# Optimization experiments

Measured on AMD Instinct MI355X. Metric: run time of the kernel, lower is better.

## Reference

```python
import jax, jax.numpy as jnp
import numpy as np

B, N, H, D, L = 4, 1024, 8, 256, 4
SVD, NSP = 16, 512
DK = D // H
EPS = 1e-6


def setup_inputs() -> dict:
    key = jax.random.key(0)
    ks = jax.random.split(key, 40)
    p = {}
    p["x"] = jax.random.normal(ks[0], (B, N, D), jnp.float32)
    p["in_degrees"] = jax.random.randint(ks[1], (N,), 0, N)
    p["out_degrees"] = jax.random.randint(ks[2], (N,), 0, N)
    p["spatial_pos"] = jax.random.randint(ks[3], (N, N), 0, NSP)
    p["svd_emb"] = jax.random.normal(ks[4], (N, 2 * SVD), jnp.float32)
    # embedding tables (padding_idx=0 -> zero row)
    p["in_deg_emb"] = (0.02 * jax.random.normal(ks[5], (N, D), jnp.float32)).at[0].set(0.0)
    p["out_deg_emb"] = (0.02 * jax.random.normal(ks[6], (N, D), jnp.float32)).at[0].set(0.0)
    p["spatial_emb"] = (0.02 * jax.random.normal(ks[7], (NSP, H), jnp.float32)).at[0].set(0.0)
    # SVD linear (stored [in, out]; y = x @ W + b)
    p["W_svd"] = 0.02 * jax.random.normal(ks[8], (2 * SVD, D), jnp.float32)
    p["b_svd"] = jnp.zeros((D,), jnp.float32)
    # per-layer stacked transformer params
    names = ["Wq", "Wk", "Wv", "Wa", "W1", "W2"]
    for i, nm in enumerate(names):
        p[nm] = 0.05 * jax.random.normal(ks[9 + i], (L, D, D), jnp.float32)
    for nm in ["bq", "bk", "bv", "ba", "b1", "b2", "ln1_b", "ln2_b"]:
        p[nm] = jnp.zeros((L, D), jnp.float32)
    p["ln1_g"] = jnp.ones((L, D), jnp.float32)
    p["ln2_g"] = jnp.ones((L, D), jnp.float32)
    return p


def _ln(x, g, b):
    mu = jnp.mean(x, axis=-1, keepdims=True)
    var = jnp.mean(jnp.square(x - mu), axis=-1, keepdims=True)
    return (x - mu) * jax.lax.rsqrt(var + EPS) * g + b


def _forward(x, svd_emb, W_svd, b_svd, in_deg_emb, out_deg_emb, spatial_emb,
             Wq, bq, Wk, bk, Wv, bv, Wa, ba, ln1_g, ln1_b,
             W1, b1, W2, b2, ln2_g, ln2_b,
             in_degrees, out_degrees, spatial_pos):
    # node-level: degree embeddings ([N,D] broadcasts over batch)
    x = x + in_deg_emb[in_degrees] + out_deg_emb[out_degrees]
    # node-level: SVD embedding (deterministic sign = +1 -> concat(u, -v))
    pos = jnp.concatenate([svd_emb[:, :SVD], -svd_emb[:, SVD:]], axis=-1)
    x = x + pos @ W_svd + b_svd
    # attention-level spatial bias: [N,N,H] -> [H,N,N], broadcast over batch
    attn_bias = jnp.transpose(spatial_emb[spatial_pos], (2, 0, 1))
    scale = 1.0 / jnp.sqrt(jnp.asarray(DK, x.dtype))

    def body(h, params):
        wq, bq_, wk, bk_, wv, bv_, wa, ba_, g1, b1_, w1, bb1, w2, bb2, g2, b2_ = params
        q = (h @ wq + bq_).reshape(B, N, H, DK)
        k = (h @ wk + bk_).reshape(B, N, H, DK)
        v = (h @ wv + bv_).reshape(B, N, H, DK)
        # scores [B,H,N,N] + spatial bias [H,N,N]
        scores = jnp.einsum('bqhd,bkhd->bhqk', q, k) * scale + attn_bias
        attn = jax.nn.softmax(scores, axis=-1)
        o = jnp.einsum('bhqk,bkhd->bqhd', attn, v).reshape(B, N, D)
        h = _ln(h + o @ wa + ba_, g1, b1_)
        f = jnp.maximum(h @ w1 + bb1, 0.0) @ w2 + bb2
        h = _ln(h + f, g2, b2_)
        return h, None

    x, _ = jax.lax.scan(body, x, (Wq, bq, Wk, bk, Wv, bv, Wa, ba, ln1_g, ln1_b,
                                  W1, b1, W2, b2, ln2_g, ln2_b))
    return x


def reference(x, svd_emb, W_svd, b_svd, in_deg_emb, out_deg_emb, spatial_emb,
              Wq, bq, Wk, bk, Wv, bv, Wa, ba, ln1_g, ln1_b,
              W1, b1, W2, b2, ln2_g, ln2_b,
              in_degrees, out_degrees, spatial_pos):
    return _forward(x, svd_emb, W_svd, b_svd, in_deg_emb, out_deg_emb, spatial_emb,
                    Wq, bq, Wk, bk, Wv, bv, Wa, ba, ln1_g, ln1_b,
                    W1, b1, W2, b2, ln2_g, ln2_b,
                    in_degrees, out_degrees, spatial_pos)
```

## Files before the change

### kernel.cpp

```cpp
#include <hip/hip_runtime.h>
#include <hip/hip_bf16.h>
#include <math.h>

#define NN 1024
#define BB 4
#define HH 8
#define DD 256
#define LL 4
#define DKK 32
#define MM 4096
#define EPSF 1e-6f

typedef __attribute__((ext_vector_type(8))) short short8;
typedef __attribute__((ext_vector_type(4))) float f32x4;

__device__ __forceinline__ unsigned short f2bf(float f) {
    __hip_bfloat16 h = __float2bfloat16(f);
    return *(unsigned short*)&h;
}
__device__ __forceinline__ float bf2f(unsigned short u) {
    unsigned v = ((unsigned)u) << 16;
    return __builtin_bit_cast(float, v);
}

__global__ __launch_bounds__(256) void init_kernel(
    const float* __restrict__ x, const int* __restrict__ deg_in,
    const int* __restrict__ deg_out, const float* __restrict__ svd,
    const float* __restrict__ in_emb, const float* __restrict__ out_emb,
    const float* __restrict__ Wsvd, const float* __restrict__ bsvd,
    const float* __restrict__ Wq, const float* __restrict__ Wk,
    const float* __restrict__ Wv, const float* __restrict__ Wa,
    const float* __restrict__ W1, const float* __restrict__ W2,
    const int* __restrict__ sp, const float* __restrict__ spemb,
    float* __restrict__ h, short* __restrict__ hb,
    short* __restrict__ Wt, short* __restrict__ bsw)
{
    int blk = blockIdx.x;
    int tid = threadIdx.x;
    {
        int n = blk & (NN - 1);
        int di = deg_in[n], dou = deg_out[n];
        float acc = x[(size_t)blk * DD + tid] + in_emb[(size_t)di * DD + tid]
                  + out_emb[(size_t)dou * DD + tid] + bsvd[tid];
        const float* sv = &svd[n * 32];
#pragma unroll
        for (int j = 0; j < 32; ++j) {
            float v = sv[j];
            v = (j < 16) ? v : -v;
            acc += v * Wsvd[j * DD + tid];
        }
        h[(size_t)blk * DD + tid] = acc;
        hb[(size_t)blk * DD + tid] = (short)f2bf(acc);
    }
    if (blk < 384) {
        __shared__ float t[64][65];
        int z = blk >> 4, tile = blk & 15;
        int name = z >> 2;
        const float* srcs[6] = {Wq, Wk, Wv, Wa, W1, W2};
        const float* W = srcs[name] + (size_t)(z & 3) * DD * DD;
        short* dst = Wt + (size_t)z * DD * DD;
        int r0 = (tile >> 2) * 64, c0 = (tile & 3) * 64;
#pragma unroll
        for (int i = 0; i < 16; ++i) {
            int idx = i * 256 + tid;
            int r = idx >> 6, cc = idx & 63;
            t[r][cc] = W[(size_t)(r0 + r) * DD + c0 + cc];
        }
        __syncthreads();
#pragma unroll
        for (int i = 0; i < 16; ++i) {
            int idx = i * 256 + tid;
            int n = idx >> 6, k = idx & 63;
            dst[(size_t)(c0 + n) * DD + r0 + k] = (short)f2bf(t[k][n]);
        }
    } else if (blk < 640) {
        int tt = (blk - 384) * 256 + tid;
        int ln = tt & 63, kt = (tt >> 6) & 15, q16 = tt >> 10;
        int qd = ln >> 4, cc = ln & 15;
        unsigned buf[8][8];
#pragma unroll
        for (int j = 0; j < 16; ++j) {
            int f = j >> 2, r = j & 3;
            int row = q16 * 16 + qd * 4 + r;
            int col = kt * 64 + f * 16 + cc;
            int pp = sp[row * NN + col];
#pragma unroll
            for (int hh = 0; hh < 8; ++hh) {
                unsigned short u = f2bf(spemb[pp * 8 + hh]);
                if (j & 1) buf[hh][j >> 1] |= ((unsigned)u) << 16;
                else       buf[hh][j >> 1] = u;
            }
        }
#pragma unroll
        for (int hh = 0; hh < 8; ++hh) {
            uint4* dst = (uint4*)&bsw[(((size_t)hh * 64 + q16) * 16 + kt) * 1024 + (size_t)ln * 16];
            dst[0] = make_uint4(buf[hh][0], buf[hh][1], buf[hh][2], buf[hh][3]);
            dst[1] = make_uint4(buf[hh][4], buf[hh][5], buf[hh][6], buf[hh][7]);
        }
    }
}

__global__ __launch_bounds__(256) void gemm_qkv_kernel(
    const short* __restrict__ A,
    const short* __restrict__ Wtq, const short* __restrict__ Wtk,
    const short* __restrict__ Wtv,
    const float* __restrict__ bq, const float* __restrict__ bk,
    const float* __restrict__ bv,
    short* __restrict__ qo, short* __restrict__ ko, short* __restrict__ vo)
{
    int z = blockIdx.z;
    const short* Wt = (z == 0) ? Wtq : (z == 1) ? Wtk : Wtv;
    const float* bs = (z == 0) ? bq : (z == 1) ? bk : bv;
    int tid = threadIdx.x, wave = tid >> 6, lane = tid & 63;
    int quad = lane >> 4, c = lane & 15;
    int m0 = blockIdx.x * 16;
    int n0 = blockIdx.y * 64 + wave * 16;
    f32x4 acc = {0.f, 0.f, 0.f, 0.f};
    const short* Ap = &A[(size_t)(m0 + c) * DD];
#pragma unroll
    for (int ks = 0; ks < 8; ++ks) {
        short8 af = *(const short8*)&Ap[ks * 32 + quad * 8];
        short8 bf = *(const short8*)&Wt[(size_t)(n0 + c) * DD + ks * 32 + quad * 8];
        acc = __builtin_amdgcn_mfma_f32_16x16x32_bf16(af, bf, acc, 0, 0, 0);
    }
    int b = m0 >> 10;
    int tok0 = (m0 & (NN - 1)) + quad * 4;
    int col = n0 + c;
    int head = col >> 5, dk = col & 31;
    int bh = b * 8 + head;
    float bv2 = bs[col];
    const float scale = 0.17677669529663687f;
    if (z == 2) {
        ushort4 pk;
        pk.x = f2bf(acc[0] + bv2); pk.y = f2bf(acc[1] + bv2);
        pk.z = f2bf(acc[2] + bv2); pk.w = f2bf(acc[3] + bv2);
        *(ushort4*)&vo[((size_t)bh * DKK + dk) * NN + tok0] = pk;
    } else {
        short* out = (z == 0) ? qo : ko;
        float sc = (z == 0) ? scale : 1.0f;
#pragma unroll
        for (int r = 0; r < 4; ++r)
            out[((size_t)bh * NN + tok0 + r) * DKK + dk] =
                (short)f2bf((acc[r] + bv2) * sc);
    }
}

template <int QKV>
__global__ __launch_bounds__(512) void layer_kernel(
    const short* __restrict__ q, const short* __restrict__ k,
    const short* __restrict__ vt, const short* __restrict__ bsw,
    const short* __restrict__ Wta, const short* __restrict__ Wt1,
    const short* __restrict__ Wt2,
    const float* __restrict__ ba, const float* __restrict__ b1,
    const float* __restrict__ b2,
    const float* __restrict__ g1, const float* __restrict__ lb1,
    const float* __restrict__ g2, const float* __restrict__ lb2,
    float* __restrict__ h,
    const short* __restrict__ Wtqn, const short* __restrict__ Wtkn,
    const short* __restrict__ Wtvn,
    const float* __restrict__ bqn, const float* __restrict__ bkn,
    const float* __restrict__ bvn,
    short* __restrict__ qo, short* __restrict__ ko, short* __restrict__ vo)
{
    int tid = threadIdx.x, wave = tid >> 6, lane = tid & 63;
    int quad = lane >> 4, c = lane & 15;
    int m0 = blockIdx.x * 16;
    int b = m0 >> 10;
    int q0 = m0 & (NN - 1);
    int qt_idx = q0 >> 4;
    int head = wave;
    int bh = b * 8 + head;
    int nb = wave * 32;

    __shared__ short Pl[8][16][72];
    __shared__ short t_in[16][264];
    __shared__ short t1s[16][264];
    __shared__ float shs[8][16][2];
    const f32x4 zero = {0.f, 0.f, 0.f, 0.f};

    {
        short (*P)[72] = Pl[wave];
        short8 qf = *(const short8*)&q[((size_t)bh * NN + q0 + c) * DKK + quad * 8];
        float m_i[4], l_i[4];
        f32x4 Oa0 = zero, Oa1 = zero;
#pragma unroll
        for (int r = 0; r < 4; ++r) { m_i[r] = -1e30f; l_i[r] = 0.f; }

        for (int kti = 0; kti < 16; ++kti) {
            int kt = kti * 64;
            f32x4 s[4];
#pragma unroll
            for (int f = 0; f < 4; ++f) {
                short8 kf = *(const short8*)&k[((size_t)bh * NN + kt + f * 16 + c) * DKK + quad * 8];
                s[f] = __builtin_amdgcn_mfma_f32_16x16x32_bf16(qf, kf, zero, 0, 0, 0);
            }
            const short* bp = &bsw[(((size_t)head * 64 + qt_idx) * 16 + kti) * 1024 + (size_t)lane * 16];
            short8 b0 = *(const short8*)bp;
            short8 b1v = *(const short8*)(bp + 8);
#pragma unroll
            for (int f = 0; f < 4; ++f)
#pragma unroll
                for (int r = 0; r < 4; ++r) {
                    int jj = f * 4 + r;
                    unsigned short uu = (unsigned short)((jj < 8) ? b0[jj] : b1v[jj - 8]);
                    s[f][r] += bf2f(uu);
                }
#pragma unroll
            for (int r = 0; r < 4; ++r) {
                float mt2 = fmaxf(fmaxf(s[0][r], s[1][r]), fmaxf(s[2][r], s[3][r]));
#pragma unroll
                for (int off = 1; off < 16; off <<= 1) mt2 = fmaxf(mt2, __shfl_xor(mt2, off));
                float mn = fmaxf(m_i[r], mt2);
                float alpha = __expf(m_i[r] - mn);
                m_i[r] = mn;
                float rs = 0.f;
#pragma unroll
                for (int f = 0; f < 4; ++f) {
                    float pr = __expf(s[f][r] - mn);
                    s[f][r] = pr;
                    rs += pr;
                }
#pragma unroll
                for (int off = 1; off < 16; off <<= 1) rs += __shfl_xor(rs, off);
                l_i[r] = l_i[r] * alpha + rs;
                Oa0[r] *= alpha;
                Oa1[r] *= alpha;
            }
#pragma unroll
            for (int f = 0; f < 4; ++f)
#pragma unroll
                for (int r = 0; r < 4; ++r)
                    P[quad * 4 + r][f * 16 + c] = (short)f2bf(s[f][r]);
#pragma unroll
            for (int kc = 0; kc < 2; ++kc) {
                short8 pf = *(const short8*)&P[c][kc * 32 + quad * 8];
                short8 vf0 = *(const short8*)&vt[((size_t)bh * DKK + 0  + c) * NN + kt + kc * 32 + quad * 8];
                short8 vf1 = *(const short8*)&vt[((size_t)bh * DKK + 16 + c) * NN + kt + kc * 32 + quad * 8];
                Oa0 = __builtin_amdgcn_mfma_f32_16x16x32_bf16(pf, vf0, Oa0, 0, 0, 0);
                Oa1 = __builtin_amdgcn_mfma_f32_16x16x32_bf16(pf, vf1, Oa1, 0, 0, 0);
            }
        }
#pragma unroll
        for (int r = 0; r < 4; ++r) {
            float invl = 1.0f / l_i[r];
            int rr = quad * 4 + r;
            t_in[rr][head * 32 + c]      = (short)f2bf(Oa0[r] * invl);
            t_in[rr][head * 32 + 16 + c] = (short)f2bf(Oa1[r] * invl);
        }
    }
    __syncthreads();

    f32x4 acc[2] = {zero, zero};
#pragma unroll
    for (int ks = 0; ks < 8; ++ks) {
        short8 af = *(const short8*)&t_in[c][ks * 32 + quad * 8];
#pragma unroll
        for (int f = 0; f < 2; ++f) {
            short8 bf = *(const short8*)&Wta[(size_t)(nb + f * 16 + c) * DD + ks * 32 + quad * 8];
            acc[f] = __builtin_amdgcn_mfma_f32_16x16x32_bf16(af, bf, acc[f], 0, 0, 0);
        }
    }
    float val[2][4];
    float ps[4] = {0.f,0.f,0.f,0.f}, ps2[4] = {0.f,0.f,0.f,0.f};
#pragma unroll
    for (int f = 0; f < 2; ++f) {
        int col = nb + f * 16 + c;
        float bv = ba[col];
#pragma unroll
        for (int r = 0; r < 4; ++r) {
            float v = h[(size_t)(m0 + quad * 4 + r) * DD + col] + acc[f][r] + bv;
            val[f][r] = v;
            ps[r] += v;
            ps2[r] += v * v;
        }
    }
#pragma unroll
    for (int r = 0; r < 4; ++r)
#pragma unroll
        for (int off = 1; off < 16; off <<= 1) {
            ps[r]  += __shfl_xor(ps[r], off);
            ps2[r] += __shfl_xor(ps2[r], off);
        }
    if (c == 0)
#pragma unroll
        for (int r = 0; r < 4; ++r) {
            shs[wave][quad * 4 + r][0] = ps[r];
            shs[wave][quad * 4 + r][1] = ps2[r];
        }
    __syncthreads();
    float res[2][4];
#pragma unroll
    for (int r = 0; r < 4; ++r) {
        int rr = quad * 4 + r;
        float ts = 0.f, t2 = 0.f;
#pragma unroll
        for (int w = 0; w < 8; ++w) { ts += shs[w][rr][0]; t2 += shs[w][rr][1]; }
        float mu = ts * (1.0f / DD);
        float rv = rsqrtf(t2 * (1.0f / DD) - mu * mu + EPSF);
#pragma unroll
        for (int f = 0; f < 2; ++f) {
            int col = nb + f * 16 + c;
            float nv = (val[f][r] - mu) * rv * g1[col] + lb1[col];
            res[f][r] = nv;
            t_in[rr][col] = (short)f2bf(nv);
        }
    }
    __syncthreads();
#pragma unroll
    for (int f = 0; f < 2; ++f) {
        int n0 = nb + f * 16;
        f32x4 a1 = zero;
#pragma unroll
        for (int ks = 0; ks < 8; ++ks) {
            short8 af = *(const short8*)&t_in[c][ks * 32 + quad * 8];
            short8 bf = *(const short8*)&Wt1[(size_t)(n0 + c) * DD + ks * 32 + quad * 8];
            a1 = __builtin_amdgcn_mfma_f32_16x16x32_bf16(af, bf, a1, 0, 0, 0);
        }
        float bv = b1[n0 + c];
#pragma unroll
        for (int r = 0; r < 4; ++r)
            t1s[quad * 4 + r][n0 + c] = (short)f2bf(fmaxf(a1[r] + bv, 0.f));
    }
    __syncthreads();
    f32x4 acc2[2] = {zero, zero};
#pragma unroll
    for (int ks = 0; ks < 8; ++ks) {
        short8 af = *(const short8*)&t1s[c][ks * 32 + quad * 8];
#pragma unroll
        for (int f = 0; f < 2; ++f) {
            short8 bf = *(const short8*)&Wt2[(size_t)(nb + f * 16 + c) * DD + ks * 32 + quad * 8];
            acc2[f] = __builtin_amdgcn_mfma_f32_16x16x32_bf16(af, bf, acc2[f], 0, 0, 0);
        }
    }
    float ps_2[4] = {0.f,0.f,0.f,0.f}, ps2_2[4] = {0.f,0.f,0.f,0.f};
#pragma unroll
    for (int f = 0; f < 2; ++f) {
        int col = nb + f * 16 + c;
        float bv = b2[col];
#pragma unroll
        for (int r = 0; r < 4; ++r) {
            float v = res[f][r] + acc2[f][r] + bv;
            val[f][r] = v;
            ps_2[r] += v;
            ps2_2[r] += v * v;
        }
    }
#pragma unroll
    for (int r = 0; r < 4; ++r)
#pragma unroll
        for (int off = 1; off < 16; off <<= 1) {
            ps_2[r]  += __shfl_xor(ps_2[r], off);
            ps2_2[r] += __shfl_xor(ps2_2[r], off);
        }
    __syncthreads();
    if (c == 0)
#pragma unroll
        for (int r = 0; r < 4; ++r) {
            shs[wave][quad * 4 + r][0] = ps_2[r];
            shs[wave][quad * 4 + r][1] = ps2_2[r];
        }
    __syncthreads();
#pragma unroll
    for (int r = 0; r < 4; ++r) {
        int rr = quad * 4 + r;
        float ts = 0.f, t2 = 0.f;
#pragma unroll
        for (int w = 0; w < 8; ++w) { ts += shs[w][rr][0]; t2 += shs[w][rr][1]; }
        float mu = ts * (1.0f / DD);
        float rv = rsqrtf(t2 * (1.0f / DD) - mu * mu + EPSF);
#pragma unroll
        for (int f = 0; f < 2; ++f) {
            int col = nb + f * 16 + c;
            float nv = (val[f][r] - mu) * rv * g2[col] + lb2[col];
            h[(size_t)(m0 + rr) * DD + col] = nv;
            t_in[rr][col] = (short)f2bf(nv);
        }
    }
    if (QKV == 0) return;
    __syncthreads();
    {
        int tok0 = q0 + quad * 4;
        const short* Wz[3]  = {Wtqn, Wtkn, Wtvn};
        const float* bz[3]  = {bqn, bkn, bvn};
        const float scale = 0.17677669529663687f;
#pragma unroll
        for (int z = 0; z < 3; ++z) {
#pragma unroll
            for (int f = 0; f < 2; ++f) {
                int n0 = nb + f * 16;
                f32x4 aq = zero;
#pragma unroll
                for (int ks = 0; ks < 8; ++ks) {
                    short8 af = *(const short8*)&t_in[c][ks * 32 + quad * 8];
                    short8 bf = *(const short8*)&Wz[z][(size_t)(n0 + c) * DD + ks * 32 + quad * 8];
                    aq = __builtin_amdgcn_mfma_f32_16x16x32_bf16(af, bf, aq, 0, 0, 0);
                }
                int col = n0 + c;
                int hd = col >> 5, dk = col & 31;
                int bh2 = b * 8 + hd;
                float bv2 = bz[z][col];
                if (z == 2) {
                    ushort4 pk;
                    pk.x = f2bf(aq[0] + bv2); pk.y = f2bf(aq[1] + bv2);
                    pk.z = f2bf(aq[2] + bv2); pk.w = f2bf(aq[3] + bv2);
                    *(ushort4*)&vo[((size_t)bh2 * DKK + dk) * NN + tok0] = pk;
                } else {
                    short* out = (z == 0) ? qo : ko;
                    float sc = (z == 0) ? scale : 1.0f;
#pragma unroll
                    for (int r = 0; r < 4; ++r)
                        out[((size_t)bh2 * NN + tok0 + r) * DKK + dk] =
                            (short)f2bf((aq[r] + bv2) * sc);
                }
            }
        }
    }
}

extern "C" void kernel_launch(void* const* d_in, const int* in_sizes, int n_in,
                              void* d_out, int out_size, void* d_ws, size_t ws_size,
                              hipStream_t stream)
{
    const float* x       = (const float*)d_in[0];
    const int*   deg_in  = (const int*)d_in[1];
    const int*   deg_out = (const int*)d_in[2];
    const int*   sp      = (const int*)d_in[3];
    const float* svd     = (const float*)d_in[4];
    const float* in_emb  = (const float*)d_in[5];
    const float* out_emb = (const float*)d_in[6];
    const float* spemb   = (const float*)d_in[7];
    const float* Wsvd    = (const float*)d_in[8];
    const float* bsvd    = (const float*)d_in[9];
    const float* Wq = (const float*)d_in[10];
    const float* Wk = (const float*)d_in[11];
    const float* Wv = (const float*)d_in[12];
    const float* Wa = (const float*)d_in[13];
    const float* W1 = (const float*)d_in[14];
    const float* W2 = (const float*)d_in[15];
    const float* bq = (const float*)d_in[16];
    const float* bk = (const float*)d_in[17];
    const float* bv = (const float*)d_in[18];
    const float* ba = (const float*)d_in[19];
    const float* b1 = (const float*)d_in[20];
    const float* b2 = (const float*)d_in[21];
    const float* ln1b = (const float*)d_in[22];
    const float* ln2b = (const float*)d_in[23];
    const float* ln1g = (const float*)d_in[24];
    const float* ln2g = (const float*)d_in[25];

    float* h = (float*)d_out;
    char*  ws = (char*)d_ws;
    short* bias = (short*)ws;
    short* qb   = (short*)(ws + ((size_t)16 << 20));
    short* kb   = (short*)(ws + ((size_t)18 << 20));
    short* vtb  = (short*)(ws + ((size_t)20 << 20));
    short* hb   = (short*)(ws + ((size_t)26 << 20));
    short* Wt   = (short*)(ws + ((size_t)28 << 20));

    init_kernel<<<MM, 256, 0, stream>>>(x, deg_in, deg_out, svd, in_emb,
        out_emb, Wsvd, bsvd, Wq, Wk, Wv, Wa, W1, W2, sp, spemb, h, hb, Wt, bias);

    const size_t WSZ = (size_t)DD * DD;
    gemm_qkv_kernel<<<dim3(MM / 16, 4, 3), 256, 0, stream>>>(
        hb, Wt + 0 * WSZ, Wt + 4 * WSZ, Wt + 8 * WSZ, bq, bk, bv, qb, kb, vtb);

    for (int l = 0; l < LL; ++l) {
        const size_t bo = (size_t)l * DD;
        const short* Wta = Wt + (3 * 4 + l) * WSZ;
        const short* Wt1 = Wt + (4 * 4 + l) * WSZ;
        const short* Wt2 = Wt + (5 * 4 + l) * WSZ;

        if (l < LL - 1) {
            const size_t bo_n = (size_t)(l + 1) * DD;
            layer_kernel<1><<<MM / 16, 512, 0, stream>>>(
                qb, kb, vtb, bias, Wta, Wt1, Wt2,
                ba + bo, b1 + bo, b2 + bo,
                ln1g + bo, ln1b + bo, ln2g + bo, ln2b + bo, h,
                Wt + (0 * 4 + l + 1) * WSZ, Wt + (1 * 4 + l + 1) * WSZ,
                Wt + (2 * 4 + l + 1) * WSZ,
                bq + bo_n, bk + bo_n, bv + bo_n, qb, kb, vtb);
        } else {
            layer_kernel<0><<<MM / 16, 512, 0, stream>>>(
                qb, kb, vtb, bias, Wta, Wt1, Wt2,
                ba + bo, b1 + bo, b2 + bo,
                ln1g + bo, ln1b + bo, ln2g + bo, ln2b + bo, h,
                nullptr, nullptr, nullptr, nullptr, nullptr, nullptr,
                nullptr, nullptr, nullptr);
        }
    }
}
```

Baseline: 352.2 us.

## Split attention KV range across two waves per head and double block size

The layer kernel now launches 1024 threads (16 waves) per block instead of 512. Each head's attention is split across two waves, each covering half the key tiles, and the partial results are merged through shared memory with a flash-style max/sum rescale. The following GEMM and LayerNorm phases give each wave 16 output columns instead of 32, and shared memory is reused through one aliased buffer. The aim is more parallelism and latency hiding per row tile in the sequential attention loop. The cost is an extra merge step with more barriers, plus higher register pressure from the 1024-thread launch bound and the fully unrolled loop.

```diff
diff --git a/kernel.cpp b/kernel.cpp
--- a/kernel.cpp
+++ b/kernel.cpp
@@ -146,7 +146,7 @@
 }
 
 template <int QKV>
-__global__ __launch_bounds__(512) void layer_kernel(
+__global__ __launch_bounds__(1024) void layer_kernel(
     const short* __restrict__ q, const short* __restrict__ k,
     const short* __restrict__ vt, const short* __restrict__ bsw,
     const short* __restrict__ Wta, const short* __restrict__ Wt1,
@@ -168,25 +168,25 @@
     int b = m0 >> 10;
     int q0 = m0 & (NN - 1);
     int qt_idx = q0 >> 4;
-    int head = wave;
-    int bh = b * 8 + head;
-    int nb = wave * 32;
-
-    __shared__ short Pl[8][16][72];
-    __shared__ short t_in[16][264];
-    __shared__ short t1s[16][264];
-    __shared__ float shs[8][16][2];
+    int nb = wave * 16;
+
+    __shared__ __align__(16) char smem[47360];
+    short (*t_in)[264] = (short(*)[264])(smem + 38912);
     const f32x4 zero = {0.f, 0.f, 0.f, 0.f};
 
     {
-        short (*P)[72] = Pl[wave];
+        int head = wave >> 1, half = wave & 1;
+        int bh = b * 8 + head;
+        short (*P)[72] = (short(*)[72])(smem + wave * 2304);
         short8 qf = *(const short8*)&q[((size_t)bh * NN + q0 + c) * DKK + quad * 8];
         float m_i[4], l_i[4];
         f32x4 Oa0 = zero, Oa1 = zero;
 #pragma unroll
         for (int r = 0; r < 4; ++r) { m_i[r] = -1e30f; l_i[r] = 0.f; }
 
-        for (int kti = 0; kti < 16; ++kti) {
+#pragma unroll
+        for (int j = 0; j < 8; ++j) {
+            int kti = half * 8 + j;
             int kt = kti * 64;
             f32x4 s[4];
 #pragma unroll
@@ -240,124 +240,133 @@
                 Oa1 = __builtin_amdgcn_mfma_f32_16x16x32_bf16(pf, vf1, Oa1, 0, 0, 0);
             }
         }
+        __syncthreads();
+        float* Om = (float*)smem;
+        float* Ml = (float*)(smem + 36864);
+        if (c == 0)
+#pragma unroll
+            for (int r = 0; r < 4; ++r) {
+                Ml[(wave * 16 + quad * 4 + r) * 2]     = m_i[r];
+                Ml[(wave * 16 + quad * 4 + r) * 2 + 1] = l_i[r];
+            }
 #pragma unroll
         for (int r = 0; r < 4; ++r) {
-            float invl = 1.0f / l_i[r];
-            int rr = quad * 4 + r;
-            t_in[rr][head * 32 + c]      = (short)f2bf(Oa0[r] * invl);
-            t_in[rr][head * 32 + 16 + c] = (short)f2bf(Oa1[r] * invl);
-        }
-    }
-    __syncthreads();
-
-    f32x4 acc[2] = {zero, zero};
+            Om[wave * 528 + (quad * 4 + r) * 33 + c]      = Oa0[r];
+            Om[wave * 528 + (quad * 4 + r) * 33 + 16 + c] = Oa1[r];
+        }
+        __syncthreads();
+        int hd2 = tid >> 7, r2 = (tid >> 3) & 15, cs = tid & 7;
+        int w0 = hd2 * 2, w1 = w0 + 1;
+        float mA = Ml[(w0 * 16 + r2) * 2], lA = Ml[(w0 * 16 + r2) * 2 + 1];
+        float mB = Ml[(w1 * 16 + r2) * 2], lB = Ml[(w1 * 16 + r2) * 2 + 1];
+        float mg = fmaxf(mA, mB);
+        float sA = __expf(mA - mg), sB = __expf(mB - mg);
+        float inv = 1.0f / (lA * sA + lB * sB);
+#pragma unroll
+        for (int cc = 0; cc < 4; ++cc) {
+            int col = cs * 4 + cc;
+            float o = Om[w0 * 528 + r2 * 33 + col] * sA
+                    + Om[w1 * 528 + r2 * 33 + col] * sB;
+            t_in[r2][hd2 * 32 + col] = (short)f2bf(o * inv);
+        }
+    }
+    __syncthreads();
+
+    float* shs = (float*)(smem + 36864);
+    f32x4 acc = zero;
 #pragma unroll
     for (int ks = 0; ks < 8; ++ks) {
         short8 af = *(const short8*)&t_in[c][ks * 32 + quad * 8];
-#pragma unroll
-        for (int f = 0; f < 2; ++f) {
-            short8 bf = *(const short8*)&Wta[(size_t)(nb + f * 16 + c) * DD + ks * 32 + quad * 8];
-            acc[f] = __builtin_amdgcn_mfma_f32_16x16x32_bf16(af, bf, acc[f], 0, 0, 0);
-        }
-    }
-    float val[2][4];
-    float ps[4] = {0.f,0.f,0.f,0.f}, ps2[4] = {0.f,0.f,0.f,0.f};
-#pragma unroll
-    for (int f = 0; f < 2; ++f) {
-        int col = nb + f * 16 + c;
+        short8 bf = *(const short8*)&Wta[(size_t)(nb + c) * DD + ks * 32 + quad * 8];
+        acc = __builtin_amdgcn_mfma_f32_16x16x32_bf16(af, bf, acc, 0, 0, 0);
+    }
+    int col = nb + c;
+    float val[4];
+    float ps = 0.f, ps2 = 0.f;
+    {
         float bv = ba[col];
 #pragma unroll
         for (int r = 0; r < 4; ++r) {
-            float v = h[(size_t)(m0 + quad * 4 + r) * DD + col] + acc[f][r] + bv;
-            val[f][r] = v;
-            ps[r] += v;
-            ps2[r] += v * v;
-        }
-    }
+            float v = h[(size_t)(m0 + quad * 4 + r) * DD + col] + acc[r] + bv;
+            val[r] = v;
+        }
+    }
+    float psr[4], ps2r[4];
+#pragma unroll
+    for (int r = 0; r < 4; ++r) { psr[r] = val[r]; ps2r[r] = val[r] * val[r]; }
 #pragma unroll
     for (int r = 0; r < 4; ++r)
 #pragma unroll
         for (int off = 1; off < 16; off <<= 1) {
-            ps[r]  += __shfl_xor(ps[r], off);
-            ps2[r] += __shfl_xor(ps2[r], off);
+            psr[r]  += __shfl_xor(psr[r], off);
+            ps2r[r] += __shfl_xor(ps2r[r], off);
         }
     if (c == 0)
 #pragma unroll
         for (int r = 0; r < 4; ++r) {
-            shs[wave][quad * 4 + r][0] = ps[r];
-            shs[wave][quad * 4 + r][1] = ps2[r];
-        }
-    __syncthreads();
-    float res[2][4];
+            shs[(wave * 16 + quad * 4 + r) * 2]     = psr[r];
+            shs[(wave * 16 + quad * 4 + r) * 2 + 1] = ps2r[r];
+        }
+    __syncthreads();
+    float res[4];
 #pragma unroll
     for (int r = 0; r < 4; ++r) {
         int rr = quad * 4 + r;
         float ts = 0.f, t2 = 0.f;
 #pragma unroll
-        for (int w = 0; w < 8; ++w) { ts += shs[w][rr][0]; t2 += shs[w][rr][1]; }
+        for (int w = 0; w < 16; ++w) {
+            ts += shs[(w * 16 + rr) * 2];
+            t2 += shs[(w * 16 + rr) * 2 + 1];
+        }
         float mu = ts * (1.0f / DD);
         float rv = rsqrtf(t2 * (1.0f / DD) - mu * mu + EPSF);
-#pragma unroll
-        for (int f = 0; f < 2; ++f) {
-            int col = nb + f * 16 + c;
-            float nv = (val[f][r] - mu) * rv * g1[col] + lb1[col];
-            res[f][r] = nv;
-            t_in[rr][col] = (short)f2bf(nv);
-        }
-    }
-    __syncthreads();
-#pragma unroll
-    for (int f = 0; f < 2; ++f) {
-        int n0 = nb + f * 16;
+        float nv = (val[r] - mu) * rv * g1[col] + lb1[col];
+        res[r] = nv;
+        t_in[rr][col] = (short)f2bf(nv);
+    }
+    __syncthreads();
+    short (*t1s)[264] = (short(*)[264])smem;
+    {
         f32x4 a1 = zero;
 #pragma unroll
         for (int ks = 0; ks < 8; ++ks) {
             short8 af = *(const short8*)&t_in[c][ks * 32 + quad * 8];
-            short8 bf = *(const short8*)&Wt1[(size_t)(n0 + c) * DD + ks * 32 + quad * 8];
+            short8 bf = *(const short8*)&Wt1[(size_t)(nb + c) * DD + ks * 32 + quad * 8];
             a1 = __builtin_amdgcn_mfma_f32_16x16x32_bf16(af, bf, a1, 0, 0, 0);
         }
-        float bv = b1[n0 + c];
+        float bv = b1[col];
 #pragma unroll
         for (int r = 0; r < 4; ++r)
-            t1s[quad * 4 + r][n0 + c] = (short)f2bf(fmaxf(a1[r] + bv, 0.f));
-    }
-    __syncthreads();
-    f32x4 acc2[2] = {zero, zero};
+            t1s[quad * 4 + r][col] = (short)f2bf(fmaxf(a1[r] + bv, 0.f));
+    }
+    __syncthreads();
+    f32x4 acc2 = zero;
 #pragma unroll
     for (int ks = 0; ks < 8; ++ks) {
         short8 af = *(const short8*)&t1s[c][ks * 32 + quad * 8];
-#pragma unroll
-        for (int f = 0; f < 2; ++f) {
-            short8 bf = *(const short8*)&Wt2[(size_t)(nb + f * 16 + c) * DD + ks * 32 + quad * 8];
-            acc2[f] = __builtin_amdgcn_mfma_f32_16x16x32_bf16(af, bf, acc2[f], 0, 0, 0);
-        }
-    }
-    float ps_2[4] = {0.f,0.f,0.f,0.f}, ps2_2[4] = {0.f,0.f,0.f,0.f};
-#pragma unroll
-    for (int f = 0; f < 2; ++f) {
-        int col = nb + f * 16 + c;
+        short8 bf = *(const short8*)&Wt2[(size_t)(nb + c) * DD + ks * 32 + quad * 8];
+        acc2 = __builtin_amdgcn_mfma_f32_16x16x32_bf16(af, bf, acc2, 0, 0, 0);
+    }
+    {
         float bv = b2[col];
 #pragma unroll
+        for (int r = 0; r < 4; ++r) val[r] = res[r] + acc2[r] + bv;
+    }
+#pragma unroll
+    for (int r = 0; r < 4; ++r) { psr[r] = val[r]; ps2r[r] = val[r] * val[r]; }
+#pragma unroll
+    for (int r = 0; r < 4; ++r)
+#pragma unroll
+        for (int off = 1; off < 16; off <<= 1) {
+            psr[r]  += __shfl_xor(psr[r], off);
+            ps2r[r] += __shfl_xor(ps2r[r], off);
+        }
+    __syncthreads();
+    if (c == 0)
+#pragma unroll
         for (int r = 0; r < 4; ++r) {
-            float v = res[f][r] + acc2[f][r] + bv;
-            val[f][r] = v;
-            ps_2[r] += v;
-            ps2_2[r] += v * v;
-        }
-    }
-#pragma unroll
-    for (int r = 0; r < 4; ++r)
-#pragma unroll
-        for (int off = 1; off < 16; off <<= 1) {
-            ps_2[r]  += __shfl_xor(ps_2[r], off);
-            ps2_2[r] += __shfl_xor(ps2_2[r], off);
-        }
-    __syncthreads();
-    if (c == 0)
-#pragma unroll
-        for (int r = 0; r < 4; ++r) {
-            shs[wave][quad * 4 + r][0] = ps_2[r];
-            shs[wave][quad * 4 + r][1] = ps2_2[r];
+            shs[(wave * 16 + quad * 4 + r) * 2]     = psr[r];
+            shs[(wave * 16 + quad * 4 + r) * 2 + 1] = ps2r[r];
         }
     __syncthreads();
 #pragma unroll
@@ -365,53 +374,47 @@
         int rr = quad * 4 + r;
         float ts = 0.f, t2 = 0.f;
 #pragma unroll
-        for (int w = 0; w < 8; ++w) { ts += shs[w][rr][0]; t2 += shs[w][rr][1]; }
+        for (int w = 0; w < 16; ++w) {
+            ts += shs[(w * 16 + rr) * 2];
+            t2 += shs[(w * 16 + rr) * 2 + 1];
+        }
         float mu = ts * (1.0f / DD);
         float rv = rsqrtf(t2 * (1.0f / DD) - mu * mu + EPSF);
-#pragma unroll
-        for (int f = 0; f < 2; ++f) {
-            int col = nb + f * 16 + c;
-            float nv = (val[f][r] - mu) * rv * g2[col] + lb2[col];
-            h[(size_t)(m0 + rr) * DD + col] = nv;
-            t_in[rr][col] = (short)f2bf(nv);
-        }
+        float nv = (val[r] - mu) * rv * g2[col] + lb2[col];
+        h[(size_t)(m0 + rr) * DD + col] = nv;
+        t_in[rr][col] = (short)f2bf(nv);
     }
     if (QKV == 0) return;
     __syncthreads();
     {
         int tok0 = q0 + quad * 4;
+        int hd = col >> 5, dk = col & 31;
+        int bh2 = b * 8 + hd;
         const short* Wz[3]  = {Wtqn, Wtkn, Wtvn};
         const float* bz[3]  = {bqn, bkn, bvn};
         const float scale = 0.17677669529663687f;
 #pragma unroll
         for (int z = 0; z < 3; ++z) {
-#pragma unroll
-            for (int f = 0; f < 2; ++f) {
-                int n0 = nb + f * 16;
-                f32x4 aq = zero;
-#pragma unroll
-                for (int ks = 0; ks < 8; ++ks) {
-                    short8 af = *(const short8*)&t_in[c][ks * 32 + quad * 8];
-                    short8 bf = *(const short8*)&Wz[z][(size_t)(n0 + c) * DD + ks * 32 + quad * 8];
-                    aq = __builtin_amdgcn_mfma_f32_16x16x32_bf16(af, bf, aq, 0, 0, 0);
-                }
-                int col = n0 + c;
-                int hd = col >> 5, dk = col & 31;
-                int bh2 = b * 8 + hd;
-                float bv2 = bz[z][col];
-                if (z == 2) {
-                    ushort4 pk;
-                    pk.x = f2bf(aq[0] + bv2); pk.y = f2bf(aq[1] + bv2);
-                    pk.z = f2bf(aq[2] + bv2); pk.w = f2bf(aq[3] + bv2);
-                    *(ushort4*)&vo[((size_t)bh2 * DKK + dk) * NN + tok0] = pk;
-                } else {
-                    short* out = (z == 0) ? qo : ko;
-                    float sc = (z == 0) ? scale : 1.0f;
-#pragma unroll
-                    for (int r = 0; r < 4; ++r)
-                        out[((size_t)bh2 * NN + tok0 + r) * DKK + dk] =
-                            (short)f2bf((aq[r] + bv2) * sc);
-                }
+            f32x4 aq = zero;
+#pragma unroll
+            for (int ks = 0; ks < 8; ++ks) {
+                short8 af = *(const short8*)&t_in[c][ks * 32 + quad * 8];
+                short8 bf = *(const short8*)&Wz[z][(size_t)(nb + c) * DD + ks * 32 + quad * 8];
+                aq = __builtin_amdgcn_mfma_f32_16x16x32_bf16(af, bf, aq, 0, 0, 0);
+            }
+            float bv2 = bz[z][col];
+            if (z == 2) {
+                ushort4 pk;
+                pk.x = f2bf(aq[0] + bv2); pk.y = f2bf(aq[1] + bv2);
+                pk.z = f2bf(aq[2] + bv2); pk.w = f2bf(aq[3] + bv2);
+                *(ushort4*)&vo[((size_t)bh2 * DKK + dk) * NN + tok0] = pk;
+            } else {
+                short* out = (z == 0) ? qo : ko;
+                float sc = (z == 0) ? scale : 1.0f;
+#pragma unroll
+                for (int r = 0; r < 4; ++r)
+                    out[((size_t)bh2 * NN + tok0 + r) * DKK + dk] =
+                        (short)f2bf((aq[r] + bv2) * sc);
             }
         }
     }
@@ -472,7 +475,7 @@
 
         if (l < LL - 1) {
             const size_t bo_n = (size_t)(l + 1) * DD;
-            layer_kernel<1><<<MM / 16, 512, 0, stream>>>(
+            layer_kernel<1><<<MM / 16, 1024, 0, stream>>>(
                 qb, kb, vtb, bias, Wta, Wt1, Wt2,
                 ba + bo, b1 + bo, b2 + bo,
                 ln1g + bo, ln1b + bo, ln2g + bo, ln2b + bo, h,
@@ -480,7 +483,7 @@
                 Wt + (2 * 4 + l + 1) * WSZ,
                 bq + bo_n, bk + bo_n, bv + bo_n, qb, kb, vtb);
         } else {
-            layer_kernel<0><<<MM / 16, 512, 0, stream>>>(
+            layer_kernel<0><<<MM / 16, 1024, 0, stream>>>(
                 qb, kb, vtb, bias, Wta, Wt1, Wt2,
                 ba + bo, b1 + bo, b2 + bo,
                 ln1g + bo, ln1b + bo, ln2g + bo, ln2b + bo, h,
```

Result: slower. 388.9 us (+10.4%).
